# Kernel tuning notes

Hardware: AMD Instinct MI355X
Metric: run time of the kernel (lower is better)

Reference implementation:

```python
import jax, jax.numpy as jnp
import numpy as np

B, C, T, D = 256, 2, 25, 4096
H = 512          # LSTM units (num_features)
H1 = 128         # fc1 hidden
NC = 2           # num_classes
LEAKY_ALPHA = 0.2  # tf.nn.leaky_relu default


def setup_inputs() -> dict:
    key = jax.random.key(0)
    ks = jax.random.split(key, 8)
    return {
        "x": jax.random.normal(ks[0], (B, C, T, D), dtype=jnp.float32),
        "kernel": jax.random.normal(ks[1], (D, 4 * H), dtype=jnp.float32) * 0.02,
        "rec_kernel": jax.random.normal(ks[2], (H, 4 * H), dtype=jnp.float32) * 0.02,
        "bias": jax.random.normal(ks[3], (4 * H,), dtype=jnp.float32) * 0.02,
        "w1": jax.random.normal(ks[4], (H, H1), dtype=jnp.float32) * 0.05,
        "b1": jax.random.normal(ks[5], (H1,), dtype=jnp.float32) * 0.05,
        "w2": jax.random.normal(ks[6], (H1, NC), dtype=jnp.float32) * 0.05,
        "b2": jax.random.normal(ks[7], (NC,), dtype=jnp.float32) * 0.05,
    }


def _lstm(xc, kernel, rec_kernel, bias):
    # xc: [B, T, D]; Keras gate order i, f, c(g), o
    h = xc.shape[0], rec_kernel.shape[0]
    zx = jnp.einsum('btd,dg->btg', xc, kernel) + bias      # [B, T, 4H]
    zx_t = jnp.swapaxes(zx, 0, 1)                           # [T, B, 4H]
    nH = rec_kernel.shape[0]
    h0 = jnp.zeros((xc.shape[0], nH), dtype=xc.dtype)
    c0 = jnp.zeros((xc.shape[0], nH), dtype=xc.dtype)

    def step(carry, z_in):
        h, c = carry
        z = z_in + h @ rec_kernel                           # [B, 4H]
        i, f, g, o = jnp.split(z, 4, axis=-1)
        i = jax.nn.sigmoid(i)
        f = jax.nn.sigmoid(f)
        g = jnp.tanh(g)
        o = jax.nn.sigmoid(o)
        c = f * c + i * g
        h = o * jnp.tanh(c)
        return (h, c), None

    (hT, _), _ = jax.lax.scan(step, (h0, c0), zx_t)
    return hT                                               # [B, H]


def reference(x, kernel, rec_kernel, bias, w1, b1, w2, b2):
    xc = x[:, 0]                                            # rgb channel (ix=0)
    h = _lstm(xc, kernel, rec_kernel, bias)
    y = jax.nn.leaky_relu(h @ w1 + b1, negative_slope=LEAKY_ALPHA)
    # dropout inactive at inference (training=False)
    return jax.nn.softmax(y @ w2 + b2, axis=-1)             # [B, NC]
```

## Files before the change

### kernel.cpp

```cpp
#include <hip/hip_runtime.h>


typedef __bf16 bf16x8 __attribute__((ext_vector_type(8)));
typedef float  f32x4  __attribute__((ext_vector_type(4)));

#define MFMA16(a, b, c) __builtin_amdgcn_mfma_f32_16x16x32_bf16((a), (b), (c), 0, 0, 0)

__device__ __forceinline__ float sigmf(float x) {
  return 1.0f / (1.0f + __expf(-x));
}
__device__ __forceinline__ float tanhf_(float x) {
  float a = fabsf(x);
  float e = __expf(-2.0f * a);
  float r = (1.0f - e) / (1.0f + e);
  return copysignf(r, x);
}

__device__ __forceinline__ void async16(__bf16* lds, const __bf16* g) {
  __builtin_amdgcn_global_load_lds(
      (const __attribute__((address_space(1))) unsigned int*)g,
      (__attribute__((address_space(3))) unsigned int*)lds, 16, 0, 0);
}

__global__ __launch_bounds__(256) void conv_xb(const float* __restrict__ x,
                                               __bf16* __restrict__ xb) {
  long o = ((long)blockIdx.x * 256 + threadIdx.x) * 8;
  int m = (int)(o >> 12);
  int k = (int)(o & 4095);
  int b = m / 25, t = m - b * 25;
  const float* src = x + (long)b * 204800 + (long)t * 4096 + k;
  f32x4 v0 = *(const f32x4*)src;
  f32x4 v1 = *(const f32x4*)(src + 4);
  bf16x8 r;
  r[0] = (__bf16)v0[0]; r[1] = (__bf16)v0[1];
  r[2] = (__bf16)v0[2]; r[3] = (__bf16)v0[3];
  r[4] = (__bf16)v1[0]; r[5] = (__bf16)v1[1];
  r[6] = (__bf16)v1[2]; r[7] = (__bf16)v1[3];
  *(bf16x8*)(xb + o) = r;
}

__global__ __launch_bounds__(256) void conv_wkT(const float* __restrict__ wk,
                                                __bf16* __restrict__ wkT) {
  __shared__ float tile[64][65];
  const int k0 = blockIdx.y * 64;
  const int n0 = blockIdx.x * 64;
  const int tx = threadIdx.x & 63;
  const int ty = threadIdx.x >> 6;
#pragma unroll
  for (int p = 0; p < 16; ++p) {
    int kr = ty + p * 4;
    tile[kr][tx] = wk[(long)(k0 + kr) * 2048 + n0 + tx];
  }
  __syncthreads();
#pragma unroll
  for (int p = 0; p < 16; ++p) {
    int nr = ty + p * 4;
    wkT[(long)(n0 + nr) * 4096 + k0 + tx] = (__bf16)tile[tx][nr];
  }
}

__global__ __launch_bounds__(256) void conv_recF2(const float* __restrict__ rec,
                                                  __bf16* __restrict__ recF) {
  __shared__ float tile[512][17];
  const int tid = threadIdx.x;
  const int g  = blockIdx.x >> 5;
  const int jt = blockIdx.x & 31;
#pragma unroll 4
  for (int p = 0; p < 32; ++p) {
    int k = (p << 4) + (tid >> 4);
    tile[k][tid & 15] = rec[(long)k * 2048 + (g << 9) + (jt << 4) + (tid & 15)];
  }
  __syncthreads();
  const int l = tid & 63;
  const int w = tid >> 6;
  long obase = ((long)((g * 32 + jt) * 16)) * 512;
#pragma unroll
  for (int q = 0; q < 4; ++q) {
    int ks = (w << 2) + q;
    bf16x8 v;
#pragma unroll
    for (int i = 0; i < 8; ++i)
      v[i] = (__bf16)tile[(ks << 5) + ((l >> 4) << 3) + i][l & 15];
    *(bf16x8*)(recF + obase + (long)ks * 512 + l * 8) = v;
  }
}

__global__ __launch_bounds__(256) void gemm_bf16(const __bf16* __restrict__ A,
                                                 const __bf16* __restrict__ Bt,
                                                 const float* __restrict__ bias,
                                                 float* __restrict__ zxr) {
  __shared__ __bf16 As[128 * 64];
  __shared__ __bf16 Bs[128 * 64];
  const int tid  = threadIdx.x;
  const int wid  = tid >> 6;
  const int lane = tid & 63;

  const int bid = blockIdx.x;
  const int swz = (bid & 7) * 100 + (bid >> 3);
  const int m0 = (swz >> 4) << 7;
  const int n0 = (swz & 15) << 7;

  const int srow  = (wid << 3) + (lane >> 3);
  const int skoff = (lane & 7) << 3;

  const int wr   = (wid >> 1) << 6;
  const int wc   = (wid & 1) << 6;
  const int lrow = lane & 15;
  const int lk8  = (lane >> 4) << 3;

  f32x4 acc[4][4];
#pragma unroll
  for (int i = 0; i < 4; ++i)
#pragma unroll
    for (int jj = 0; jj < 4; ++jj) {
      f32x4 z = {0.f, 0.f, 0.f, 0.f};
      acc[i][jj] = z;
    }

  const __bf16* Ag = A  + (long)(m0 + srow) * 4096 + skoff;
  const __bf16* Bg = Bt + (long)(n0 + srow) * 4096 + skoff;
  __bf16* Al = &As[(wid << 3) * 64];
  __bf16* Bl = &Bs[(wid << 3) * 64];

  for (int k0 = 0; k0 < 4096; k0 += 64) {
    __syncthreads();
#pragma unroll
    for (int q = 0; q < 4; ++q) {
      async16(Al + q * (32 * 64), Ag + (long)(q * 32) * 4096 + k0);
      async16(Bl + q * (32 * 64), Bg + (long)(q * 32) * 4096 + k0);
    }
    __syncthreads();
#pragma unroll
    for (int kk = 0; kk < 2; ++kk) {
      bf16x8 af[4], bv[4];
#pragma unroll
      for (int fr = 0; fr < 4; ++fr)
        af[fr] = *(const bf16x8*)&As[(wr + fr * 16 + lrow) * 64 + (kk << 5) + lk8];
#pragma unroll
      for (int fc = 0; fc < 4; ++fc)
        bv[fc] = *(const bf16x8*)&Bs[(wc + fc * 16 + lrow) * 64 + (kk << 5) + lk8];
#pragma unroll
      for (int fr = 0; fr < 4; ++fr)
#pragma unroll
        for (int fc = 0; fc < 4; ++fc)
          acc[fr][fc] = MFMA16(af[fr], bv[fc], acc[fr][fc]);
    }
  }

  const int mlow = (lane >> 4) << 2;
#pragma unroll
  for (int fc = 0; fc < 4; ++fc) {
    int n = n0 + wc + fc * 16 + lrow;
    float bvs = bias[n];
#pragma unroll
    for (int fr = 0; fr < 4; ++fr) {
      int mb = m0 + wr + fr * 16 + mlow;
#pragma unroll
      for (int r = 0; r < 4; ++r) {
        int m = mb + r;
        int b = m / 25;
        int tt = m - b * 25;
        zxr[((long)((tt << 8) + b) << 11) + n] = acc[fr][fc][r] + bvs;
      }
    }
  }
}

__global__ __launch_bounds__(256) void lstm_persist(const float* __restrict__ zxr,
                                                    const __bf16* __restrict__ recF,
                                                    __bf16* __restrict__ hA,
                                                    __bf16* __restrict__ hB,
                                                    __bf16* __restrict__ hplain,
                                                    int* bar) {
  __shared__ __bf16 recS[32768];
  const int tid  = threadIdx.x;
  const int wid  = tid >> 6;
  const int lane = tid & 63;
  const int bid  = blockIdx.x;
  const int jt   = bid & 31;
  const int rtg  = bid >> 5;
  const int rt   = (rtg << 2) + wid;

  {
    const __bf16* src = recF + (long)(jt << 4) * 512;
#pragma unroll
    for (int g = 0; g < 4; ++g)
#pragma unroll
      for (int q = 0; q < 4; ++q)
        *(bf16x8*)(recS + g * 8192 + q * 2048 + tid * 8) =
            *(const bf16x8*)(src + (long)g * 262144 + q * 2048 + tid * 8);
  }

  const int j    = (jt << 4) + (lane & 15);
  const int mlow = (lane >> 4) << 2;
  const int ks2  = j >> 5;
  const int lhi  = ((j >> 3) & 3) << 4;
  const int i2   = j & 7;
  float c[4];
  int brow[4];
#pragma unroll
  for (int r = 0; r < 4; ++r) {
    c[r] = 0.f;
    brow[r] = (rt << 4) + mlow + r;
  }
  __syncthreads();

  float zv[4][4];
#pragma unroll
  for (int g = 0; g < 4; ++g)
#pragma unroll
    for (int r = 0; r < 4; ++r)
      zv[g][r] = zxr[((long)brow[r] << 11) + (g << 9) + j];

  const __bf16* hin = hA;
  __bf16* hout = hA;

  for (int t = 0; t < 25; ++t) {
    if (t > 0) {
      f32x4 acc[4];
#pragma unroll
      for (int g = 0; g < 4; ++g) {
        f32x4 z = {0.f, 0.f, 0.f, 0.f};
        acc[g] = z;
      }
#pragma unroll 4
      for (int ks = 0; ks < 16; ++ks) {
        bf16x8 a = *(const bf16x8*)(hin + ((((rt << 4) + ks) << 6) + lane) * 8);
#pragma unroll
        for (int g = 0; g < 4; ++g) {
          bf16x8 b = *(const bf16x8*)(recS + ((((g << 4) + ks) << 6) + lane) * 8);
          acc[g] = MFMA16(a, b, acc[g]);
        }
      }
#pragma unroll
      for (int g = 0; g < 4; ++g)
#pragma unroll
        for (int r = 0; r < 4; ++r)
          zv[g][r] += acc[g][r];
    }

#pragma unroll
    for (int r = 0; r < 4; ++r) {
      float ig = sigmf(zv[0][r]);
      float fg = sigmf(zv[1][r]);
      float gg = tanhf_(zv[2][r]);
      float og = sigmf(zv[3][r]);
      float cn = fg * c[r] + ig * gg;
      c[r] = cn;
      float hv = og * tanhf_(cn);
      hout[((((rt << 4) + ks2) << 6) + (lhi | (brow[r] & 15))) * 8 + i2] = (__bf16)hv;
      if (t == 24) hplain[(brow[r] << 9) + j] = (__bf16)hv;
    }

    if (t < 24) {
#pragma unroll
      for (int g = 0; g < 4; ++g)
#pragma unroll
        for (int r = 0; r < 4; ++r)
          zv[g][r] = zxr[((long)(((t + 1) << 8) + brow[r]) << 11) + (g << 9) + j];

      __syncthreads();
      if (tid == 0) {
        __hip_atomic_fetch_add(bar, 1, __ATOMIC_RELEASE, __HIP_MEMORY_SCOPE_AGENT);
        const int target = 128 * (t + 1);
        while (__hip_atomic_load(bar, __ATOMIC_ACQUIRE, __HIP_MEMORY_SCOPE_AGENT) < target)
          __builtin_amdgcn_s_sleep(2);
      }
      __syncthreads();
    }

    hin  = hout;
    hout = (t & 1) ? hA : hB;
  }
}

__global__ __launch_bounds__(128) void head_kernel(const __bf16* __restrict__ h,
                                                   const float* __restrict__ w1,
                                                   const float* __restrict__ b1,
                                                   const float* __restrict__ w2,
                                                   const float* __restrict__ b2,
                                                   float* __restrict__ out) {
  const int b = blockIdx.x;
  const int j = threadIdx.x;
  float acc = b1[j];
#pragma unroll 8
  for (int k = 0; k < 512; ++k)
    acc += (float)h[b * 512 + k] * w1[k * 128 + j];
  float y = acc > 0.f ? acc : 0.2f * acc;

  __shared__ float s0[128], s1[128];
  s0[j] = y * w2[j * 2 + 0];
  s1[j] = y * w2[j * 2 + 1];
  __syncthreads();
#pragma unroll
  for (int s = 64; s > 0; s >>= 1) {
    if (j < s) { s0[j] += s0[j + s]; s1[j] += s1[j + s]; }
    __syncthreads();
  }
  if (j == 0) {
    float l0 = s0[0] + b2[0];
    float l1 = s1[0] + b2[1];
    float m  = fmaxf(l0, l1);
    float e0 = __expf(l0 - m);
    float e1 = __expf(l1 - m);
    float inv = 1.0f / (e0 + e1);
    out[b * 2 + 0] = e0 * inv;
    out[b * 2 + 1] = e1 * inv;
  }
}

extern "C" void kernel_launch(void* const* d_in, const int* in_sizes, int n_in,
                              void* d_out, int out_size, void* d_ws, size_t ws_size,
                              hipStream_t stream) {
  const float* x    = (const float*)d_in[0];
  const float* wk   = (const float*)d_in[1];
  const float* rec  = (const float*)d_in[2];
  const float* bias = (const float*)d_in[3];
  const float* w1   = (const float*)d_in[4];
  const float* b1   = (const float*)d_in[5];
  const float* w2   = (const float*)d_in[6];
  const float* b2   = (const float*)d_in[7];
  float* out = (float*)d_out;

  char* w = (char*)d_ws;
  float*  zxr    = (float*)(w + 0);
  __bf16* xb     = (__bf16*)(w + 52428800);
  __bf16* wkT    = (__bf16*)(w + 104857600);
  __bf16* recF   = (__bf16*)(w + 121634816);
  __bf16* hA     = (__bf16*)(w + 123731968);
  __bf16* hB     = (__bf16*)(w + 123994112);
  __bf16* hplain = (__bf16*)(w + 124256256);
  int*    bar    = (int*)(w + 124518400);

  hipMemsetAsync(bar, 0, 256, stream);

  conv_xb   <<<12800, 256, 0, stream>>>(x, xb);
  conv_wkT  <<<dim3(32, 64), 256, 0, stream>>>(wk, wkT);
  conv_recF2<<<128, 256, 0, stream>>>(rec, recF);

  gemm_bf16<<<800, 256, 0, stream>>>(xb, wkT, bias, zxr);

  lstm_persist<<<128, 256, 0, stream>>>(zxr, recF, hA, hB, hplain, bar);

  head_kernel<<<256, 128, 0, stream>>>(hplain, w1, b1, w2, b2, out);
}
```

Measured before the change: 781.2 us.

## Use per-group flag barriers in LSTM and write GEMM output in natural layout

The recurrent kernel's single global atomic counter barrier is replaced by per-row-group flag arrays. Each block publishes its timestep, and 32 threads poll only the 32 blocks that share its batch rows, which reduces atomic contention and avoids waiting on unrelated groups. The GEMM epilogue now stores zx in natural row order, avoiding the per-element divide by 25 and the transposed scatter; the LSTM reads with a stride of 25 rows instead. The strided per-step reads may be less coalesced across batch rows.

```diff
diff --git a/kernel.cpp b/kernel.cpp
--- a/kernel.cpp
+++ b/kernel.cpp
@@ -88,7 +88,7 @@
 __global__ __launch_bounds__(256) void gemm_bf16(const __bf16* __restrict__ A,
                                                  const __bf16* __restrict__ Bt,
                                                  const float* __restrict__ bias,
-                                                 float* __restrict__ zxr) {
+                                                 float* __restrict__ zx) {
   __shared__ __bf16 As[128 * 64];
   __shared__ __bf16 Bs[128 * 64];
   const int tid  = threadIdx.x;
@@ -156,17 +156,13 @@
     for (int fr = 0; fr < 4; ++fr) {
       int mb = m0 + wr + fr * 16 + mlow;
 #pragma unroll
-      for (int r = 0; r < 4; ++r) {
-        int m = mb + r;
-        int b = m / 25;
-        int tt = m - b * 25;
-        zxr[((long)((tt << 8) + b) << 11) + n] = acc[fr][fc][r] + bvs;
-      }
-    }
-  }
-}
-
-__global__ __launch_bounds__(256) void lstm_persist(const float* __restrict__ zxr,
+      for (int r = 0; r < 4; ++r)
+        zx[(long)(mb + r) * 2048 + n] = acc[fr][fc][r] + bvs;
+    }
+  }
+}
+
+__global__ __launch_bounds__(256) void lstm_persist(const float* __restrict__ zx,
                                                     const __bf16* __restrict__ recF,
                                                     __bf16* __restrict__ hA,
                                                     __bf16* __restrict__ hB,
@@ -180,6 +176,7 @@
   const int jt   = bid & 31;
   const int rtg  = bid >> 5;
   const int rt   = (rtg << 2) + wid;
+  int* gbar = bar + (rtg << 6);
 
   {
     const __bf16* src = recF + (long)(jt << 4) * 512;
@@ -210,7 +207,7 @@
   for (int g = 0; g < 4; ++g)
 #pragma unroll
     for (int r = 0; r < 4; ++r)
-      zv[g][r] = zxr[((long)brow[r] << 11) + (g << 9) + j];
+      zv[g][r] = zx[(((long)brow[r] * 25) << 11) + (g << 9) + j];
 
   const __bf16* hin = hA;
   __bf16* hout = hA;
@@ -257,14 +254,16 @@
       for (int g = 0; g < 4; ++g)
 #pragma unroll
         for (int r = 0; r < 4; ++r)
-          zv[g][r] = zxr[((long)(((t + 1) << 8) + brow[r]) << 11) + (g << 9) + j];
+          zv[g][r] = zx[(((long)brow[r] * 25 + t + 1) << 11) + (g << 9) + j];
 
       __syncthreads();
-      if (tid == 0) {
-        __hip_atomic_fetch_add(bar, 1, __ATOMIC_RELEASE, __HIP_MEMORY_SCOPE_AGENT);
-        const int target = 128 * (t + 1);
-        while (__hip_atomic_load(bar, __ATOMIC_ACQUIRE, __HIP_MEMORY_SCOPE_AGENT) < target)
-          __builtin_amdgcn_s_sleep(2);
+      if (tid == 0)
+        __hip_atomic_store(&gbar[jt], t + 1, __ATOMIC_RELEASE,
+                           __HIP_MEMORY_SCOPE_AGENT);
+      if (tid < 32) {
+        while (__hip_atomic_load(&gbar[tid], __ATOMIC_ACQUIRE,
+                                 __HIP_MEMORY_SCOPE_AGENT) < t + 1)
+          __builtin_amdgcn_s_sleep(4);
       }
       __syncthreads();
     }
@@ -323,7 +322,7 @@
   float* out = (float*)d_out;
 
   char* w = (char*)d_ws;
-  float*  zxr    = (float*)(w + 0);
+  float*  zx     = (float*)(w + 0);
   __bf16* xb     = (__bf16*)(w + 52428800);
   __bf16* wkT    = (__bf16*)(w + 104857600);
   __bf16* recF   = (__bf16*)(w + 121634816);
@@ -332,15 +331,15 @@
   __bf16* hplain = (__bf16*)(w + 124256256);
   int*    bar    = (int*)(w + 124518400);
 
-  hipMemsetAsync(bar, 0, 256, stream);
+  hipMemsetAsync(bar, 0, 1024, stream);
 
   conv_xb   <<<12800, 256, 0, stream>>>(x, xb);
   conv_wkT  <<<dim3(32, 64), 256, 0, stream>>>(wk, wkT);
   conv_recF2<<<128, 256, 0, stream>>>(rec, recF);
 
-  gemm_bf16<<<800, 256, 0, stream>>>(xb, wkT, bias, zxr);
-
-  lstm_persist<<<128, 256, 0, stream>>>(zxr, recF, hA, hB, hplain, bar);
+  gemm_bf16<<<800, 256, 0, stream>>>(xb, wkT, bias, zx);
+
+  lstm_persist<<<128, 256, 0, stream>>>(zx, recF, hA, hB, hplain, bar);
 
   head_kernel<<<256, 128, 0, stream>>>(hplain, w1, b1, w2, b2, out);
 }
```

Measured after the change: 736.5 us. 1.06x faster.
